# Kernel optimization log

Hardware: AMD Instinct MI355X
Metric: run time of the kernel (lower is better)

Reference implementation:

```python
import jax, jax.numpy as jnp
import numpy as np

EPS = 1e-5

def rmsnorm(x, w):
    return x * jax.lax.rsqrt(jnp.mean(x * x, axis=-1, keepdims=True) + EPS) * w

def setup_inputs() -> dict:
    key = jax.random.key(0)
    ks = jax.random.split(key, 10)
    b, d, n, k, r, l = 64, 256, 16, 4, 16, 256
    inp = {}
    inp['x_1'] = jax.random.normal(ks[0], (b, d), jnp.float32)
    inp['x_2'] = jax.random.normal(ks[1], (b, d), jnp.float32)
    inp['norm_w'] = jnp.ones((d,), jnp.float32)
    inp['conv_w'] = jax.random.normal(ks[2], (d, 1, k), jnp.float32) * 0.2
    inp['conv_b'] = jax.random.normal(ks[3], (d,), jnp.float32) * 0.02
    inp['in_w'] = jax.random.normal(ks[4], (2 * d, d), jnp.float32) * 0.02
    inp['xproj_w'] = jax.random.normal(ks[5], (r + 2 * n, d), jnp.float32) * 0.02
    inp['dt_w'] = jax.random.normal(ks[6], (d, r), jnp.float32) * 0.02
    inp['dt_b'] = jax.random.normal(ks[7], (d,), jnp.float32) * 0.02
    inp['out_w'] = jax.random.normal(ks[8], (d, d), jnp.float32) * 0.02
    # A = repeat(arange(1, n+1), 'n -> d n'); A_log = log(A)
    inp['A_log'] = jnp.tile(jnp.log(jnp.arange(1, n + 1, dtype=jnp.float32)), (d, 1))
    inp['D'] = jnp.ones((d,), jnp.float32)
    inp['l'] = l
    return inp

def _dwconv(x, conv_w, conv_b, l):
    # x: (b, l, d); depthwise causal-ish conv with padding k-1 on both sides, truncate to l
    d = x.shape[-1]
    k = conv_w.shape[-1]
    xt = x.transpose(0, 2, 1)  # (b, d, l)
    out = jax.lax.conv_general_dilated(
        xt, conv_w, window_strides=(1,), padding=[(k - 1, k - 1)],
        dimension_numbers=('NCH', 'OIH', 'NCH'), feature_group_count=d)
    out = out[:, :, :l] + conv_b[None, :, None]
    return out.transpose(0, 2, 1)  # (b, l, d)

def reference(x_1, x_2, norm_w, conv_w, conv_b, in_w, xproj_w, dt_w, dt_b, out_w, A_log, D, l):
    b, d = x_1.shape
    n = A_log.shape[1]
    r = dt_w.shape[1]
    # RMSNorm then broadcast along sequence
    x1 = jnp.broadcast_to(rmsnorm(x_1, norm_w)[:, None, :], (b, l, d))
    x2 = jnp.broadcast_to(rmsnorm(x_2, norm_w)[:, None, :], (b, l, d))
    # in_proj (no bias), split into x and res
    xr1 = x1 @ in_w.T
    x1c, res1 = xr1[..., :d], xr1[..., d:]
    xr2 = x2 @ in_w.T
    x2c, _ = xr2[..., :d], xr2[..., d:]
    # depthwise conv + silu
    x1s = jax.nn.silu(_dwconv(x1c, conv_w, conv_b, l))
    x2s = jax.nn.silu(_dwconv(x2c, conv_w, conv_b, l))
    # ssm: delta/B/C from x2s, scanned input u = x1s
    A = -jnp.exp(A_log)  # (d, n)
    xdbl = x2s @ xproj_w.T  # (b, l, r + 2n)
    delta, B, C = xdbl[..., :r], xdbl[..., r:r + n], xdbl[..., r + n:]
    delta = jax.nn.softplus(delta @ dt_w.T + dt_b)  # (b, l, d)
    deltaA = jnp.exp(jnp.einsum('bld,dn->bldn', delta, A))  # (b, l, d, n)
    dBu = (delta * x1s)[..., None] * B[:, :, None, :]  # (b, l, d, n)
    def step(h, inputs):
        dA_i, dBu_i, C_i = inputs  # (b,d,n), (b,d,n), (b,n)
        h = dA_i * h + dBu_i
        y = jnp.einsum('bdn,bn->bd', h, C_i)
        return h, y
    h0 = jnp.zeros((b, d, n), x1s.dtype)
    _, ys = jax.lax.scan(step, h0, (deltaA.transpose(1, 0, 2, 3),
                                     dBu.transpose(1, 0, 2, 3),
                                     C.transpose(1, 0, 2)))
    y = ys.transpose(1, 0, 2) + x1s * D  # (b, l, d)
    y = y * jax.nn.silu(res1)
    out = rmsnorm(y @ out_w.T, norm_w)
    return out[:, -1, :]
```

## Files before the change

kernel.cpp:

```cpp
#include <hip/hip_runtime.h>
#include <math.h>

#define D 256
#define N 16
#define R 16

#define WS_X1C  0
#define WS_RES1 16384
#define WS_X2C  32768

__device__ __forceinline__ float silu_f(float x) { return x / (1.0f + expf(-x)); }
__device__ __forceinline__ float softplus_f(float x) {
    return fmaxf(x, 0.0f) + log1pf(expf(-fabsf(x)));
}

__global__ __launch_bounds__(1024) void k1_inw(
    const float* __restrict__ x1_in, const float* __restrict__ x2_in,
    const float* __restrict__ norm_w, const float* __restrict__ in_w,
    float* __restrict__ ws)
{
    __shared__ float s_n1[D];
    __shared__ float s_n2[D];
    __shared__ float s_red[8];
    const int t  = threadIdx.x;
    const int b  = blockIdx.x >> 2;
    const int cc = blockIdx.x & 3;
    const int q8 = t & 7;
    const int r8 = t >> 3;
    const int row = cc * 128 + r8;
    const bool dual = (cc < 2);

    const float* __restrict__ wr = in_w + (size_t)row * D;
    float4 w[8];
    #pragma unroll
    for (int k = 0; k < 8; ++k) w[k] = *(const float4*)(wr + 4 * q8 + 32 * k);

    float v1 = 0.0f, v2 = 0.0f;
    if (t < D) {
        v1 = x1_in[b * D + t];
        float p1 = v1 * v1, p2 = 0.0f;
        if (dual) { v2 = x2_in[b * D + t]; p2 = v2 * v2; }
        #pragma unroll
        for (int off = 32; off >= 1; off >>= 1) {
            p1 += __shfl_down(p1, off, 64);
            p2 += __shfl_down(p2, off, 64);
        }
        if ((t & 63) == 0) { s_red[t >> 6] = p1; s_red[4 + (t >> 6)] = p2; }
    }
    __syncthreads();
    if (t < D) {
        const float ss1 = s_red[0] + s_red[1] + s_red[2] + s_red[3];
        const float wn = norm_w[t];
        s_n1[t] = v1 * rsqrtf(ss1 * (1.0f / D) + 1e-5f) * wn;
        if (dual) {
            const float ss2 = s_red[4] + s_red[5] + s_red[6] + s_red[7];
            s_n2[t] = v2 * rsqrtf(ss2 * (1.0f / D) + 1e-5f) * wn;
        }
    }
    __syncthreads();

    float a1 = 0.0f, a2 = 0.0f;
    #pragma unroll
    for (int k = 0; k < 8; ++k) {
        const int e = 4 * q8 + 32 * k;
        const float4 n4 = *(const float4*)(s_n1 + e);
        a1 += w[k].x*n4.x + w[k].y*n4.y + w[k].z*n4.z + w[k].w*n4.w;
        if (dual) {
            const float4 m4 = *(const float4*)(s_n2 + e);
            a2 += w[k].x*m4.x + w[k].y*m4.y + w[k].z*m4.z + w[k].w*m4.w;
        }
    }
    a1 += __shfl_xor(a1, 1, 64); a1 += __shfl_xor(a1, 2, 64); a1 += __shfl_xor(a1, 4, 64);
    if (dual) {
        a2 += __shfl_xor(a2, 1, 64); a2 += __shfl_xor(a2, 2, 64); a2 += __shfl_xor(a2, 4, 64);
    }
    if (q8 == 0) {
        if (dual) {
            ws[WS_X1C + b * D + row] = a1;
            ws[WS_X2C + b * D + row] = a2;
        } else {
            ws[WS_RES1 + b * D + (row - 256)] = a1;
        }
    }
}

__global__ __launch_bounds__(1024) void k2_rest(
    const float* __restrict__ conv_w, const float* __restrict__ conv_b,
    const float* __restrict__ xproj_w, const float* __restrict__ dt_w,
    const float* __restrict__ dt_b, const float* __restrict__ A_log,
    const float* __restrict__ Dp, const int* __restrict__ l_ptr,
    const float* __restrict__ out_w, const float* __restrict__ norm_w,
    const float* __restrict__ ws, float* __restrict__ out)
{
    __shared__ float s_x2s[4][D];
    __shared__ float s_xdbl[192];
    __shared__ float s_y[D];
    __shared__ float s_z[D];
    __shared__ float s_red[4];
    const int b = blockIdx.x;
    const int t = threadIdx.x;
    const int q   = t & 3;
    const int dot = t >> 2;
    const int l = *l_ptr;

    float x1c = 0.0f, x2c = 0.0f, res1 = 0.0f, cb = 0.0f, dtb = 0.0f,
          dpj = 0.0f, wnj = 0.0f;
    float4 cw = make_float4(0.f, 0.f, 0.f, 0.f);
    float dtr[R];
    float alog[N];
    if (t < D) {
        x1c  = ws[WS_X1C  + b * D + t];
        x2c  = ws[WS_X2C  + b * D + t];
        res1 = ws[WS_RES1 + b * D + t];
        cw   = *(const float4*)(conv_w + 4 * t);
        cb   = conv_b[t];
        dtb  = dt_b[t];
        dpj  = Dp[t];
        wnj  = norm_w[t];
        const float* __restrict__ dtrow = dt_w + (size_t)t * R;
        #pragma unroll
        for (int qq = 0; qq < R; ++qq) dtr[qq] = dtrow[qq];
        const float* __restrict__ arow = A_log + (size_t)t * N;
        #pragma unroll
        for (int n = 0; n < N; ++n) alog[n] = arow[n];
    }
    const int xo = t >> 4;
    const int xs = t & 15;
    float4 wx[4];
    if (t < 768) {
        const float* __restrict__ pr = xproj_w + (size_t)xo * D;
        #pragma unroll
        for (int k = 0; k < 4; ++k) wx[k] = *(const float4*)(pr + 4 * xs + 64 * k);
    }
    const float* __restrict__ orow = out_w + (size_t)dot * D;
    float4 wo[8];
    #pragma unroll
    for (int k = 0; k < 8; ++k) wo[k] = *(const float4*)(orow + q * 4 + 16 * k);

    float x1s[4];
    if (t < D) {
        float ksum[4];
        ksum[0] = cw.w;
        ksum[1] = cw.z + cw.w;
        ksum[2] = cw.y + cw.z + cw.w;
        ksum[3] = cw.x + cw.y + cw.z + cw.w;
        #pragma unroll
        for (int tc = 0; tc < 4; ++tc) {
            x1s[tc] = silu_f(ksum[tc] * x1c + cb);
            s_x2s[tc][t] = silu_f(ksum[tc] * x2c + cb);
        }
    }
    __syncthreads();

    if (t < 768) {
        float acc[4] = {0.f, 0.f, 0.f, 0.f};
        #pragma unroll
        for (int k = 0; k < 4; ++k) {
            const int e = 4 * xs + 64 * k;
            #pragma unroll
            for (int tc = 0; tc < 4; ++tc) {
                const float4 x4 = *(const float4*)(&s_x2s[tc][e]);
                acc[tc] += wx[k].x*x4.x + wx[k].y*x4.y + wx[k].z*x4.z + wx[k].w*x4.w;
            }
        }
        #pragma unroll
        for (int tc = 0; tc < 4; ++tc) {
            acc[tc] += __shfl_xor(acc[tc], 1, 64);
            acc[tc] += __shfl_xor(acc[tc], 2, 64);
            acc[tc] += __shfl_xor(acc[tc], 4, 64);
            acc[tc] += __shfl_xor(acc[tc], 8, 64);
        }
        if (xs == 0) {
            #pragma unroll
            for (int tc = 0; tc < 4; ++tc) s_xdbl[tc * 48 + xo] = acc[tc];
        }
    }
    __syncthreads();

    if (t < D) {
        float delta[4];
        #pragma unroll
        for (int tc = 0; tc < 4; ++tc) {
            float acc = 0.0f;
            #pragma unroll
            for (int qq = 0; qq < R; ++qq) acc += s_xdbl[tc * 48 + qq] * dtr[qq];
            delta[tc] = softplus_f(acc + dtb);
        }
        float Aa[N];
        #pragma unroll
        for (int n = 0; n < N; ++n) Aa[n] = -expf(alog[n]);
        float h[N];
        #pragma unroll
        for (int n = 0; n < N; ++n) h[n] = 0.0f;
        const int nexp = (l < 3) ? l : 3;
        for (int tt = 0; tt < nexp; ++tt) {
            const float dl = delta[tt];
            const float du = dl * x1s[tt];
            #pragma unroll
            for (int n = 0; n < N; ++n) {
                const float dA = expf(dl * Aa[n]);
                h[n] = dA * h[n] + du * s_xdbl[tt * 48 + 16 + n];
            }
        }
        if (l > 3) {
            const float dl = delta[3];
            const float du = dl * x1s[3];
            const float steps = (float)(l - 3);
            #pragma unroll
            for (int n = 0; n < N; ++n) {
                const float z   = dl * Aa[n];
                const float em1 = expm1f(z);
                const float emN = expm1f(steps * z);
                const float ratio = (em1 != 0.0f) ? (emN / em1) : steps;
                const float pw = emN + 1.0f;
                h[n] = pw * h[n] + du * s_xdbl[3 * 48 + 16 + n] * ratio;
            }
        }
        const int fc = ((l - 1) < 3) ? (l - 1) : 3;
        float y = 0.0f;
        #pragma unroll
        for (int n = 0; n < N; ++n) y += h[n] * s_xdbl[fc * 48 + 32 + n];
        y += x1s[fc] * dpj;
        y *= silu_f(res1);
        s_y[t] = y;
    }
    __syncthreads();

    {
        float4 wo2[8];
        #pragma unroll
        for (int k = 0; k < 8; ++k)
            wo2[k] = *(const float4*)(orow + q * 4 + 16 * (8 + k));
        float acc = 0.0f;
        #pragma unroll
        for (int k = 0; k < 8; ++k) {
            const int e = q * 4 + 16 * k;
            const float4 y4 = *(const float4*)(s_y + e);
            acc += wo[k].x*y4.x + wo[k].y*y4.y + wo[k].z*y4.z + wo[k].w*y4.w;
        }
        #pragma unroll
        for (int k = 0; k < 8; ++k) {
            const int e = q * 4 + 16 * (8 + k);
            const float4 y4 = *(const float4*)(s_y + e);
            acc += wo2[k].x*y4.x + wo2[k].y*y4.y + wo2[k].z*y4.z + wo2[k].w*y4.w;
        }
        acc += __shfl_xor(acc, 1, 64);
        acc += __shfl_xor(acc, 2, 64);
        if (q == 0) s_z[dot] = acc;
    }
    __syncthreads();

    if (t < D) {
        const float zz = s_z[t];
        float p = zz * zz;
        #pragma unroll
        for (int off = 32; off >= 1; off >>= 1) p += __shfl_down(p, off, 64);
        if ((t & 63) == 0) s_red[t >> 6] = p;
    }
    __syncthreads();
    if (t < D) {
        const float ss = s_red[0] + s_red[1] + s_red[2] + s_red[3];
        out[b * D + t] = s_z[t] * rsqrtf(ss * (1.0f / D) + 1e-5f) * wnj;
    }
}

extern "C" void kernel_launch(void* const* d_in, const int* in_sizes, int n_in,
                              void* d_out, int out_size, void* d_ws, size_t ws_size,
                              hipStream_t stream) {
    const float* x1      = (const float*)d_in[0];
    const float* x2      = (const float*)d_in[1];
    const float* norm_w  = (const float*)d_in[2];
    const float* conv_w  = (const float*)d_in[3];
    const float* conv_b  = (const float*)d_in[4];
    const float* in_w    = (const float*)d_in[5];
    const float* xproj_w = (const float*)d_in[6];
    const float* dt_w    = (const float*)d_in[7];
    const float* dt_b    = (const float*)d_in[8];
    const float* out_w   = (const float*)d_in[9];
    const float* A_log   = (const float*)d_in[10];
    const float* Dp      = (const float*)d_in[11];
    const int*   l_ptr   = (const int*)d_in[12];
    float* out = (float*)d_out;
    float* ws  = (float*)d_ws;

    const int batch = in_sizes[0] / D;

    k1_inw<<<dim3(batch * 4), dim3(1024), 0, stream>>>(x1, x2, norm_w, in_w, ws);
    k2_rest<<<dim3(batch), dim3(1024), 0, stream>>>(conv_w, conv_b, xproj_w,
                                                    dt_w, dt_b, A_log, Dp, l_ptr,
                                                    out_w, norm_w, ws, out);
}
```

Baseline: 91.32 us.

## Fuse RMSNorm/in_proj kernel into the SSM kernel, keep intermediates in LDS

Merges the two launches into one kernel per batch row. The in_proj matvec for x1c, x2c and res1 is now computed in-block and stored in shared memory, so the workspace round trip and the second launch go away. In exchange each block handles all 512 in_w rows, where before 4 blocks per batch shared them, so only 64 blocks run and the per-block serial work grows.

```diff
diff --git a/kernel.cpp b/kernel.cpp
--- a/kernel.cpp
+++ b/kernel.cpp
@@ -4,119 +4,48 @@
 #define D 256
 #define N 16
 #define R 16
-
-#define WS_X1C  0
-#define WS_RES1 16384
-#define WS_X2C  32768
 
 __device__ __forceinline__ float silu_f(float x) { return x / (1.0f + expf(-x)); }
 __device__ __forceinline__ float softplus_f(float x) {
     return fmaxf(x, 0.0f) + log1pf(expf(-fabsf(x)));
 }
 
-__global__ __launch_bounds__(1024) void k1_inw(
+__global__ __launch_bounds__(1024) void fused(
     const float* __restrict__ x1_in, const float* __restrict__ x2_in,
-    const float* __restrict__ norm_w, const float* __restrict__ in_w,
-    float* __restrict__ ws)
+    const float* __restrict__ norm_w, const float* __restrict__ conv_w,
+    const float* __restrict__ conv_b, const float* __restrict__ in_w,
+    const float* __restrict__ xproj_w, const float* __restrict__ dt_w,
+    const float* __restrict__ dt_b, const float* __restrict__ A_log,
+    const float* __restrict__ Dp, const int* __restrict__ l_ptr,
+    const float* __restrict__ out_w, float* __restrict__ out)
 {
     __shared__ float s_n1[D];
     __shared__ float s_n2[D];
-    __shared__ float s_red[8];
-    const int t  = threadIdx.x;
-    const int b  = blockIdx.x >> 2;
-    const int cc = blockIdx.x & 3;
-    const int q8 = t & 7;
-    const int r8 = t >> 3;
-    const int row = cc * 128 + r8;
-    const bool dual = (cc < 2);
-
-    const float* __restrict__ wr = in_w + (size_t)row * D;
-    float4 w[8];
-    #pragma unroll
-    for (int k = 0; k < 8; ++k) w[k] = *(const float4*)(wr + 4 * q8 + 32 * k);
-
-    float v1 = 0.0f, v2 = 0.0f;
-    if (t < D) {
-        v1 = x1_in[b * D + t];
-        float p1 = v1 * v1, p2 = 0.0f;
-        if (dual) { v2 = x2_in[b * D + t]; p2 = v2 * v2; }
-        #pragma unroll
-        for (int off = 32; off >= 1; off >>= 1) {
-            p1 += __shfl_down(p1, off, 64);
-            p2 += __shfl_down(p2, off, 64);
-        }
-        if ((t & 63) == 0) { s_red[t >> 6] = p1; s_red[4 + (t >> 6)] = p2; }
-    }
-    __syncthreads();
-    if (t < D) {
-        const float ss1 = s_red[0] + s_red[1] + s_red[2] + s_red[3];
-        const float wn = norm_w[t];
-        s_n1[t] = v1 * rsqrtf(ss1 * (1.0f / D) + 1e-5f) * wn;
-        if (dual) {
-            const float ss2 = s_red[4] + s_red[5] + s_red[6] + s_red[7];
-            s_n2[t] = v2 * rsqrtf(ss2 * (1.0f / D) + 1e-5f) * wn;
-        }
-    }
-    __syncthreads();
-
-    float a1 = 0.0f, a2 = 0.0f;
-    #pragma unroll
-    for (int k = 0; k < 8; ++k) {
-        const int e = 4 * q8 + 32 * k;
-        const float4 n4 = *(const float4*)(s_n1 + e);
-        a1 += w[k].x*n4.x + w[k].y*n4.y + w[k].z*n4.z + w[k].w*n4.w;
-        if (dual) {
-            const float4 m4 = *(const float4*)(s_n2 + e);
-            a2 += w[k].x*m4.x + w[k].y*m4.y + w[k].z*m4.z + w[k].w*m4.w;
-        }
-    }
-    a1 += __shfl_xor(a1, 1, 64); a1 += __shfl_xor(a1, 2, 64); a1 += __shfl_xor(a1, 4, 64);
-    if (dual) {
-        a2 += __shfl_xor(a2, 1, 64); a2 += __shfl_xor(a2, 2, 64); a2 += __shfl_xor(a2, 4, 64);
-    }
-    if (q8 == 0) {
-        if (dual) {
-            ws[WS_X1C + b * D + row] = a1;
-            ws[WS_X2C + b * D + row] = a2;
-        } else {
-            ws[WS_RES1 + b * D + (row - 256)] = a1;
-        }
-    }
-}
-
-__global__ __launch_bounds__(1024) void k2_rest(
-    const float* __restrict__ conv_w, const float* __restrict__ conv_b,
-    const float* __restrict__ xproj_w, const float* __restrict__ dt_w,
-    const float* __restrict__ dt_b, const float* __restrict__ A_log,
-    const float* __restrict__ Dp, const int* __restrict__ l_ptr,
-    const float* __restrict__ out_w, const float* __restrict__ norm_w,
-    const float* __restrict__ ws, float* __restrict__ out)
-{
+    __shared__ float s_x1c[D];
+    __shared__ float s_x2c[D];
+    __shared__ float s_res1[D];
     __shared__ float s_x2s[4][D];
     __shared__ float s_xdbl[192];
     __shared__ float s_y[D];
     __shared__ float s_z[D];
-    __shared__ float s_red[4];
+    __shared__ float s_red[8];
+
     const int b = blockIdx.x;
     const int t = threadIdx.x;
-    const int q   = t & 3;
-    const int dot = t >> 2;
     const int l = *l_ptr;
 
-    float x1c = 0.0f, x2c = 0.0f, res1 = 0.0f, cb = 0.0f, dtb = 0.0f,
-          dpj = 0.0f, wnj = 0.0f;
+    float x1v = 0.0f, x2v = 0.0f, cb = 0.0f, dtb = 0.0f, dpj = 0.0f, wnj = 0.0f;
     float4 cw = make_float4(0.f, 0.f, 0.f, 0.f);
     float dtr[R];
     float alog[N];
     if (t < D) {
-        x1c  = ws[WS_X1C  + b * D + t];
-        x2c  = ws[WS_X2C  + b * D + t];
-        res1 = ws[WS_RES1 + b * D + t];
-        cw   = *(const float4*)(conv_w + 4 * t);
-        cb   = conv_b[t];
-        dtb  = dt_b[t];
-        dpj  = Dp[t];
-        wnj  = norm_w[t];
+        x1v = x1_in[b * D + t];
+        x2v = x2_in[b * D + t];
+        wnj = norm_w[t];
+        cw  = *(const float4*)(conv_w + 4 * t);
+        cb  = conv_b[t];
+        dtb = dt_b[t];
+        dpj = Dp[t];
         const float* __restrict__ dtrow = dt_w + (size_t)t * R;
         #pragma unroll
         for (int qq = 0; qq < R; ++qq) dtr[qq] = dtrow[qq];
@@ -124,6 +53,61 @@
         #pragma unroll
         for (int n = 0; n < N; ++n) alog[n] = arow[n];
     }
+
+    if (t < D) {
+        float p1 = x1v * x1v, p2 = x2v * x2v;
+        #pragma unroll
+        for (int off = 32; off >= 1; off >>= 1) {
+            p1 += __shfl_down(p1, off, 64);
+            p2 += __shfl_down(p2, off, 64);
+        }
+        if ((t & 63) == 0) { s_red[t >> 6] = p1; s_red[4 + (t >> 6)] = p2; }
+    }
+    __syncthreads();
+    if (t < D) {
+        const float ss1 = s_red[0] + s_red[1] + s_red[2] + s_red[3];
+        const float ss2 = s_red[4] + s_red[5] + s_red[6] + s_red[7];
+        s_n1[t] = x1v * rsqrtf(ss1 * (1.0f / D) + 1e-5f) * wnj;
+        s_n2[t] = x2v * rsqrtf(ss2 * (1.0f / D) + 1e-5f) * wnj;
+    }
+    __syncthreads();
+
+    const int q8 = t & 7;
+    const int r8 = t >> 3;
+    #pragma unroll
+    for (int p = 0; p < 2; ++p) {
+        const int row = p * 128 + r8;
+        const float* __restrict__ wr = in_w + (size_t)row * D;
+        float a1 = 0.0f, a2 = 0.0f;
+        #pragma unroll
+        for (int k = 0; k < 8; ++k) {
+            const int e = 4 * q8 + 32 * k;
+            const float4 w4 = *(const float4*)(wr + e);
+            const float4 n4 = *(const float4*)(s_n1 + e);
+            const float4 m4 = *(const float4*)(s_n2 + e);
+            a1 += w4.x*n4.x + w4.y*n4.y + w4.z*n4.z + w4.w*n4.w;
+            a2 += w4.x*m4.x + w4.y*m4.y + w4.z*m4.z + w4.w*m4.w;
+        }
+        a1 += __shfl_xor(a1, 1, 64); a1 += __shfl_xor(a1, 2, 64); a1 += __shfl_xor(a1, 4, 64);
+        a2 += __shfl_xor(a2, 1, 64); a2 += __shfl_xor(a2, 2, 64); a2 += __shfl_xor(a2, 4, 64);
+        if (q8 == 0) { s_x1c[row] = a1; s_x2c[row] = a2; }
+    }
+    #pragma unroll
+    for (int p = 0; p < 2; ++p) {
+        const int row = 256 + p * 128 + r8;
+        const float* __restrict__ wr = in_w + (size_t)row * D;
+        float a1 = 0.0f;
+        #pragma unroll
+        for (int k = 0; k < 8; ++k) {
+            const int e = 4 * q8 + 32 * k;
+            const float4 w4 = *(const float4*)(wr + e);
+            const float4 n4 = *(const float4*)(s_n1 + e);
+            a1 += w4.x*n4.x + w4.y*n4.y + w4.z*n4.z + w4.w*n4.w;
+        }
+        a1 += __shfl_xor(a1, 1, 64); a1 += __shfl_xor(a1, 2, 64); a1 += __shfl_xor(a1, 4, 64);
+        if (q8 == 0) s_res1[row - 256] = a1;
+    }
+
     const int xo = t >> 4;
     const int xs = t & 15;
     float4 wx[4];
@@ -132,13 +116,21 @@
         #pragma unroll
         for (int k = 0; k < 4; ++k) wx[k] = *(const float4*)(pr + 4 * xs + 64 * k);
     }
+    const int q   = t & 3;
+    const int dot = t >> 2;
     const float* __restrict__ orow = out_w + (size_t)dot * D;
     float4 wo[8];
     #pragma unroll
     for (int k = 0; k < 8; ++k) wo[k] = *(const float4*)(orow + q * 4 + 16 * k);
 
+    __syncthreads();
+
     float x1s[4];
-    if (t < D) {
+    float res1v = 0.0f;
+    if (t < D) {
+        const float x1cv = s_x1c[t];
+        const float x2cv = s_x2c[t];
+        res1v = s_res1[t];
         float ksum[4];
         ksum[0] = cw.w;
         ksum[1] = cw.z + cw.w;
@@ -146,8 +138,8 @@
         ksum[3] = cw.x + cw.y + cw.z + cw.w;
         #pragma unroll
         for (int tc = 0; tc < 4; ++tc) {
-            x1s[tc] = silu_f(ksum[tc] * x1c + cb);
-            s_x2s[tc][t] = silu_f(ksum[tc] * x2c + cb);
+            x1s[tc] = silu_f(ksum[tc] * x1cv + cb);
+            s_x2s[tc][t] = silu_f(ksum[tc] * x2cv + cb);
         }
     }
     __syncthreads();
@@ -221,7 +213,7 @@
         #pragma unroll
         for (int n = 0; n < N; ++n) y += h[n] * s_xdbl[fc * 48 + 32 + n];
         y += x1s[fc] * dpj;
-        y *= silu_f(res1);
+        y *= silu_f(res1v);
         s_y[t] = y;
     }
     __syncthreads();
@@ -281,12 +273,11 @@
     const float* Dp      = (const float*)d_in[11];
     const int*   l_ptr   = (const int*)d_in[12];
     float* out = (float*)d_out;
-    float* ws  = (float*)d_ws;
+    (void)d_ws; (void)ws_size; (void)n_in; (void)out_size;
 
     const int batch = in_sizes[0] / D;
 
-    k1_inw<<<dim3(batch * 4), dim3(1024), 0, stream>>>(x1, x2, norm_w, in_w, ws);
-    k2_rest<<<dim3(batch), dim3(1024), 0, stream>>>(conv_w, conv_b, xproj_w,
-                                                    dt_w, dt_b, A_log, Dp, l_ptr,
-                                                    out_w, norm_w, ws, out);
+    fused<<<dim3(batch), dim3(1024), 0, stream>>>(x1, x2, norm_w, conv_w, conv_b,
+                                                  in_w, xproj_w, dt_w, dt_b, A_log,
+                                                  Dp, l_ptr, out_w, out);
 }
```

Measured after the change: 93.95 us. 2.9% more time.

## Fuse conv+SiLU into in_proj kernel and prefetch k2 weights into L2

Applied to the files above, without the earlier changes.

Moves the depthwise-conv collapse and SiLU activations (x1s, x2s, silu(res1)) out of the second kernel and into the in_proj kernel epilogue, storing per-timestep activations in a per-batch workspace layout. The first kernel also issues dummy loads of out_w, xproj_w, dt_w and A_log so those weights sit in L2 before the second kernel reads them. This shortens the latency-bound second kernel's critical path. In exchange, the first kernel does extra loads and writes 4x more activation data to the workspace.

```diff
diff --git a/kernel.cpp b/kernel.cpp
--- a/kernel.cpp
+++ b/kernel.cpp
@@ -5,9 +5,10 @@
 #define N 16
 #define R 16
 
-#define WS_X1C  0
-#define WS_RES1 16384
-#define WS_X2C  32768
+#define WS_STRIDE 2304
+#define WS_X2S 0
+#define WS_X1S 1024
+#define WS_RES 2048
 
 __device__ __forceinline__ float silu_f(float x) { return x / (1.0f + expf(-x)); }
 __device__ __forceinline__ float softplus_f(float x) {
@@ -17,6 +18,9 @@
 __global__ __launch_bounds__(1024) void k1_inw(
     const float* __restrict__ x1_in, const float* __restrict__ x2_in,
     const float* __restrict__ norm_w, const float* __restrict__ in_w,
+    const float* __restrict__ conv_w, const float* __restrict__ conv_b,
+    const float* __restrict__ xproj_w, const float* __restrict__ dt_w,
+    const float* __restrict__ A_log, const float* __restrict__ out_w,
     float* __restrict__ ws)
 {
     __shared__ float s_n1[D];
@@ -35,6 +39,32 @@
     #pragma unroll
     for (int k = 0; k < 8; ++k) w[k] = *(const float4*)(wr + 4 * q8 + 32 * k);
 
+    float4 cwr = make_float4(0.f, 0.f, 0.f, 0.f);
+    float  cbr = 0.0f;
+    if (dual) {
+        cwr = *(const float4*)(conv_w + 4 * row);
+        cbr = conv_b[row];
+    }
+
+    {
+        const int bid = blockIdx.x;
+        float wsum = 0.0f;
+        if (t < 512) {
+            const float4 v = ((const float4*)out_w)[((bid & 31) << 9) + t];
+            wsum = v.x + v.y + v.z + v.w;
+        } else if (t < 608) {
+            const float4 v = ((const float4*)xproj_w)[(bid & 31) * 96 + (t - 512)];
+            wsum = v.x + v.y + v.z + v.w;
+        } else if (t < 672) {
+            const float4 v = ((const float4*)dt_w)[((bid & 15) << 6) + (t - 608)];
+            wsum = v.x + v.y + v.z + v.w;
+        } else if (t < 736) {
+            const float4 v = ((const float4*)A_log)[((bid & 15) << 6) + (t - 672)];
+            wsum = v.x + v.y + v.z + v.w;
+        }
+        asm volatile("" :: "v"(wsum));
+    }
+
     float v1 = 0.0f, v2 = 0.0f;
     if (t < D) {
         v1 = x1_in[b * D + t];
@@ -59,40 +89,52 @@
     }
     __syncthreads();
 
-    float a1 = 0.0f, a2 = 0.0f;
-    #pragma unroll
-    for (int k = 0; k < 8; ++k) {
-        const int e = 4 * q8 + 32 * k;
-        const float4 n4 = *(const float4*)(s_n1 + e);
-        a1 += w[k].x*n4.x + w[k].y*n4.y + w[k].z*n4.z + w[k].w*n4.w;
-        if (dual) {
+    float* __restrict__ wb = ws + (size_t)b * WS_STRIDE;
+    if (dual) {
+        float a1 = 0.0f, a2 = 0.0f;
+        #pragma unroll
+        for (int k = 0; k < 8; ++k) {
+            const int e = 4 * q8 + 32 * k;
+            const float4 n4 = *(const float4*)(s_n1 + e);
             const float4 m4 = *(const float4*)(s_n2 + e);
+            a1 += w[k].x*n4.x + w[k].y*n4.y + w[k].z*n4.z + w[k].w*n4.w;
             a2 += w[k].x*m4.x + w[k].y*m4.y + w[k].z*m4.z + w[k].w*m4.w;
         }
-    }
-    a1 += __shfl_xor(a1, 1, 64); a1 += __shfl_xor(a1, 2, 64); a1 += __shfl_xor(a1, 4, 64);
-    if (dual) {
+        a1 += __shfl_xor(a1, 1, 64); a1 += __shfl_xor(a1, 2, 64); a1 += __shfl_xor(a1, 4, 64);
         a2 += __shfl_xor(a2, 1, 64); a2 += __shfl_xor(a2, 2, 64); a2 += __shfl_xor(a2, 4, 64);
-    }
-    if (q8 == 0) {
-        if (dual) {
-            ws[WS_X1C + b * D + row] = a1;
-            ws[WS_X2C + b * D + row] = a2;
-        } else {
-            ws[WS_RES1 + b * D + (row - 256)] = a1;
-        }
+        if (q8 == 0) {
+            float ks[4];
+            ks[0] = cwr.w;
+            ks[1] = cwr.z + cwr.w;
+            ks[2] = cwr.y + cwr.z + cwr.w;
+            ks[3] = cwr.x + cwr.y + cwr.z + cwr.w;
+            #pragma unroll
+            for (int tc = 0; tc < 4; ++tc) {
+                wb[WS_X2S + tc * 256 + row] = silu_f(ks[tc] * a2 + cbr);
+                wb[WS_X1S + tc * 256 + row] = silu_f(ks[tc] * a1 + cbr);
+            }
+        }
+    } else {
+        float a1 = 0.0f;
+        #pragma unroll
+        for (int k = 0; k < 8; ++k) {
+            const int e = 4 * q8 + 32 * k;
+            const float4 n4 = *(const float4*)(s_n1 + e);
+            a1 += w[k].x*n4.x + w[k].y*n4.y + w[k].z*n4.z + w[k].w*n4.w;
+        }
+        a1 += __shfl_xor(a1, 1, 64); a1 += __shfl_xor(a1, 2, 64); a1 += __shfl_xor(a1, 4, 64);
+        if (q8 == 0) wb[WS_RES + (row - 256)] = silu_f(a1);
     }
 }
 
 __global__ __launch_bounds__(1024) void k2_rest(
-    const float* __restrict__ conv_w, const float* __restrict__ conv_b,
     const float* __restrict__ xproj_w, const float* __restrict__ dt_w,
     const float* __restrict__ dt_b, const float* __restrict__ A_log,
     const float* __restrict__ Dp, const int* __restrict__ l_ptr,
     const float* __restrict__ out_w, const float* __restrict__ norm_w,
     const float* __restrict__ ws, float* __restrict__ out)
 {
-    __shared__ float s_x2s[4][D];
+    __shared__ float s_x2s[4 * D];
     __shared__ float s_xdbl[192];
     __shared__ float s_y[D];
     __shared__ float s_z[D];
@@ -103,20 +145,19 @@
     const int dot = t >> 2;
     const int l = *l_ptr;
 
-    float x1c = 0.0f, x2c = 0.0f, res1 = 0.0f, cb = 0.0f, dtb = 0.0f,
-          dpj = 0.0f, wnj = 0.0f;
-    float4 cw = make_float4(0.f, 0.f, 0.f, 0.f);
+    const float* __restrict__ wbat = ws + (size_t)b * WS_STRIDE;
+    float x1sv[4] = {0.f, 0.f, 0.f, 0.f};
+    float res1s = 0.0f, dtb = 0.0f, dpj = 0.0f, wnj = 0.0f;
     float dtr[R];
     float alog[N];
     if (t < D) {
-        x1c  = ws[WS_X1C  + b * D + t];
-        x2c  = ws[WS_X2C  + b * D + t];
-        res1 = ws[WS_RES1 + b * D + t];
-        cw   = *(const float4*)(conv_w + 4 * t);
-        cb   = conv_b[t];
-        dtb  = dt_b[t];
-        dpj  = Dp[t];
-        wnj  = norm_w[t];
+        ((float4*)s_x2s)[t] = *(const float4*)(wbat + WS_X2S + 4 * t);
+        #pragma unroll
+        for (int tc = 0; tc < 4; ++tc) x1sv[tc] = wbat[WS_X1S + tc * 256 + t];
+        res1s = wbat[WS_RES + t];
+        dtb = dt_b[t];
+        dpj = Dp[t];
+        wnj = norm_w[t];
         const float* __restrict__ dtrow = dt_w + (size_t)t * R;
         #pragma unroll
         for (int qq = 0; qq < R; ++qq) dtr[qq] = dtrow[qq];
@@ -137,19 +178,6 @@
     #pragma unroll
     for (int k = 0; k < 8; ++k) wo[k] = *(const float4*)(orow + q * 4 + 16 * k);
 
-    float x1s[4];
-    if (t < D) {
-        float ksum[4];
-        ksum[0] = cw.w;
-        ksum[1] = cw.z + cw.w;
-        ksum[2] = cw.y + cw.z + cw.w;
-        ksum[3] = cw.x + cw.y + cw.z + cw.w;
-        #pragma unroll
-        for (int tc = 0; tc < 4; ++tc) {
-            x1s[tc] = silu_f(ksum[tc] * x1c + cb);
-            s_x2s[tc][t] = silu_f(ksum[tc] * x2c + cb);
-        }
-    }
     __syncthreads();
 
     if (t < 768) {
@@ -159,7 +187,7 @@
             const int e = 4 * xs + 64 * k;
             #pragma unroll
             for (int tc = 0; tc < 4; ++tc) {
-                const float4 x4 = *(const float4*)(&s_x2s[tc][e]);
+                const float4 x4 = *(const float4*)(&s_x2s[tc * 256 + e]);
                 acc[tc] += wx[k].x*x4.x + wx[k].y*x4.y + wx[k].z*x4.z + wx[k].w*x4.w;
             }
         }
@@ -195,7 +223,7 @@
         const int nexp = (l < 3) ? l : 3;
         for (int tt = 0; tt < nexp; ++tt) {
             const float dl = delta[tt];
-            const float du = dl * x1s[tt];
+            const float du = dl * x1sv[tt];
             #pragma unroll
             for (int n = 0; n < N; ++n) {
                 const float dA = expf(dl * Aa[n]);
@@ -204,7 +232,7 @@
         }
         if (l > 3) {
             const float dl = delta[3];
-            const float du = dl * x1s[3];
+            const float du = dl * x1sv[3];
             const float steps = (float)(l - 3);
             #pragma unroll
             for (int n = 0; n < N; ++n) {
@@ -220,8 +248,8 @@
         float y = 0.0f;
         #pragma unroll
         for (int n = 0; n < N; ++n) y += h[n] * s_xdbl[fc * 48 + 32 + n];
-        y += x1s[fc] * dpj;
-        y *= silu_f(res1);
+        y += x1sv[fc] * dpj;
+        y *= res1s;
         s_y[t] = y;
     }
     __syncthreads();
@@ -282,11 +310,14 @@
     const int*   l_ptr   = (const int*)d_in[12];
     float* out = (float*)d_out;
     float* ws  = (float*)d_ws;
+    (void)n_in; (void)out_size; (void)ws_size;
 
     const int batch = in_sizes[0] / D;
 
-    k1_inw<<<dim3(batch * 4), dim3(1024), 0, stream>>>(x1, x2, norm_w, in_w, ws);
-    k2_rest<<<dim3(batch), dim3(1024), 0, stream>>>(conv_w, conv_b, xproj_w,
-                                                    dt_w, dt_b, A_log, Dp, l_ptr,
-                                                    out_w, norm_w, ws, out);
+    k1_inw<<<dim3(batch * 4), dim3(1024), 0, stream>>>(x1, x2, norm_w, in_w,
+                                                       conv_w, conv_b, xproj_w,
+                                                       dt_w, A_log, out_w, ws);
+    k2_rest<<<dim3(batch), dim3(1024), 0, stream>>>(xproj_w, dt_w, dt_b, A_log,
+                                                    Dp, l_ptr, out_w, norm_w,
+                                                    ws, out);
 }
```

Measured after the change: 92.21 us. About the same (+1.0%).
